# Kernel optimization log

Measured on AMD Instinct MI355X. Metric: run time of the kernel, lower is better.

The kernel has to match this reference:

```python
import jax, jax.numpy as jnp
import numpy as np

B, S, IN_DIM = 8, 1024, 512
EMBED_DIM, NUM_HEADS = 512, 8
HEAD_DIM = EMBED_DIM // NUM_HEADS
LN_EPS = 1e-5


def setup_inputs() -> dict:
    key = jax.random.key(0)
    k1, k2, k3 = jax.random.split(key, 3)
    x = jax.random.normal(k1, (B, S, IN_DIM), dtype=jnp.float32)
    # xavier_uniform for qkv_proj.weight [3*embed, in] and o_proj.weight [embed, embed]
    lim_qkv = float(np.sqrt(6.0 / (3 * EMBED_DIM + IN_DIM)))
    w_qkv = jax.random.uniform(k2, (3 * EMBED_DIM, IN_DIM), dtype=jnp.float32,
                               minval=-lim_qkv, maxval=lim_qkv)
    lim_o = float(np.sqrt(6.0 / (EMBED_DIM + EMBED_DIM)))
    w_o = jax.random.uniform(k3, (EMBED_DIM, EMBED_DIM), dtype=jnp.float32,
                             minval=-lim_o, maxval=lim_o)
    return {"x": x, "w_qkv": w_qkv, "w_o": w_o}


def reference(x, w_qkv, w_o):
    b, s, _ = x.shape
    # fused QKV projection: [b, s, 3*embed]
    qkv = jnp.einsum('bsi,ei->bse', x, w_qkv)
    # [b, h, s, 3*head_dim]
    qkv = qkv.reshape(b, s, NUM_HEADS, 3 * HEAD_DIM).transpose(0, 2, 1, 3)
    q, k, v = jnp.split(qkv, 3, axis=-1)
    scale = 1.0 / np.sqrt(HEAD_DIM)
    logits = jnp.einsum('bhqd,bhkd->bhqk', q, k) * scale  # [b, h, s, s]
    attn = jax.nn.softmax(logits, axis=-1)
    vals = jnp.einsum('bhqk,bhkd->bhqd', attn, v)
    vals = vals.transpose(0, 2, 1, 3).reshape(b, s, EMBED_DIM)
    o = jnp.einsum('bse,fe->bsf', vals, w_o)
    # LayerNorm over [seq, embed] jointly (fresh nn.LayerNorm([N, D]): weight=1, bias=0)
    mu = jnp.mean(o, axis=(-2, -1), keepdims=True)
    var = jnp.var(o, axis=(-2, -1), keepdims=True)
    o = (o - mu) / jnp.sqrt(var + LN_EPS)
    return o
```

## Files before the change

kernel.cpp:

```cpp
#include <hip/hip_runtime.h>
#include <hip/hip_bf16.h>
#include <math.h>

#define BB 8
#define SS 1024
#define INDIM 512
#define ED 512
#define NH 8
#define HD 64

typedef __attribute__((ext_vector_type(8))) short short8;
typedef __attribute__((ext_vector_type(4))) float f32x4;
typedef __attribute__((ext_vector_type(16))) float f32x16;
typedef unsigned short u16;

static __device__ __forceinline__ u16 f2bf(float f) {
  union { float f; unsigned u; } v; v.f = f;
  unsigned r = v.u + 0x7fffu + ((v.u >> 16) & 1u);
  return (u16)(r >> 16);
}

static __device__ __forceinline__ unsigned cvt_pk_bf16(float a, float b) {
  unsigned r;
  asm("v_cvt_pk_bf16_f32 %0, %1, %2" : "=v"(r) : "v"(a), "v"(b));
  return r;
}
static __device__ __forceinline__ float fast_exp2(float x) {
  float r; asm("v_exp_f32 %0, %1" : "=v"(r) : "v"(x)); return r;
}

__global__ void cvt_all(const float* __restrict__ x, const float* __restrict__ wq,
                        const float* __restrict__ wo, u16* __restrict__ xb,
                        u16* __restrict__ wqb, u16* __restrict__ wob) {
  const int n1 = 1048576;
  const int n2 = n1 + 196608;
  const int n3 = n2 + 65536;
  int i = blockIdx.x * blockDim.x + threadIdx.x;
  int stride = gridDim.x * blockDim.x;
  for (; i < n3; i += stride) {
    const float4* src; ushort4* dst; int j;
    if (i < n1)      { src = (const float4*)x;  dst = (ushort4*)xb;  j = i; }
    else if (i < n2) { src = (const float4*)wq; dst = (ushort4*)wqb; j = i - n1; }
    else             { src = (const float4*)wo; dst = (ushort4*)wob; j = i - n2; }
    float4 v = src[j];
    ushort4 o;
    o.x = f2bf(v.x); o.y = f2bf(v.y); o.z = f2bf(v.z); o.w = f2bf(v.w);
    dst[j] = o;
  }
}

template<int EPI>
__global__ __launch_bounds__(256, 2)
void gemm_nt(const u16* __restrict__ A, const u16* __restrict__ Bm, int K,
             float* __restrict__ outF,
             u16* __restrict__ qws, u16* __restrict__ kws, u16* __restrict__ vtws,
             float2* __restrict__ partials)
{
  __shared__ u16 As[128][72];
  __shared__ u16 Bs[128][72];
  const int tid = threadIdx.x;
  const int lane = tid & 63;
  const int wv = tid >> 6;
  const int wr = wv >> 1, wc = wv & 1;
  const int bm = blockIdx.x, bn = blockIdx.y;
  const int l15 = lane & 15, lg = lane >> 4;

  f32x4 acc[4][4];
  #pragma unroll
  for (int i = 0; i < 4; i++)
    #pragma unroll
    for (int j = 0; j < 4; j++) acc[i][j] = (f32x4){0.f, 0.f, 0.f, 0.f};

  for (int kk = 0; kk < K; kk += 64) {
    #pragma unroll
    for (int t = 0; t < 4; t++) {
      int ci = tid + t * 256;
      int row = ci >> 3, col = (ci & 7) * 8;
      uint4 va = *(const uint4*)(A + (size_t)(bm * 128 + row) * K + kk + col);
      *(uint4*)&As[row][col] = va;
      uint4 vb = *(const uint4*)(Bm + (size_t)(bn * 128 + row) * K + kk + col);
      *(uint4*)&Bs[row][col] = vb;
    }
    __syncthreads();
    #pragma unroll
    for (int kc = 0; kc < 2; kc++) {
      short8 af[4], bf[4];
      #pragma unroll
      for (int mi = 0; mi < 4; mi++)
        af[mi] = *(const short8*)&As[wr * 64 + mi * 16 + l15][kc * 32 + lg * 8];
      #pragma unroll
      for (int ni = 0; ni < 4; ni++)
        bf[ni] = *(const short8*)&Bs[wc * 64 + ni * 16 + l15][kc * 32 + lg * 8];
      #pragma unroll
      for (int mi = 0; mi < 4; mi++)
        #pragma unroll
        for (int ni = 0; ni < 4; ni++)
          acc[mi][ni] = __builtin_amdgcn_mfma_f32_16x16x32_bf16(af[mi], bf[ni], acc[mi][ni], 0, 0, 0);
    }
    __syncthreads();
  }

  #pragma unroll
  for (int mi = 0; mi < 4; mi++) {
    int rowg = bm * 128 + wr * 64 + mi * 16 + lg * 4;
    #pragma unroll
    for (int ni = 0; ni < 4; ni++) {
      int colg = bn * 128 + wc * 64 + ni * 16 + l15;
      #pragma unroll
      for (int r = 0; r < 4; r++) {
        int rg = rowg + r;
        float v = acc[mi][ni][r];
        if (EPI == 0) {
          int b = rg >> 10, s = rg & 1023;
          int h = colg / 192, c = colg - h * 192;
          int bh = b * 8 + h;
          if (c < 64)
            qws[((size_t)(bh * 1024 + s)) * 64 + c] = f2bf(v * 0.18033688f);
          else if (c < 128)
            kws[((size_t)(bh * 1024 + s)) * 64 + (c - 64)] = f2bf(v);
          else
            vtws[((size_t)(bh * 64 + (c - 128))) * 1024 + s] = f2bf(v);
        } else {
          outF[(size_t)rg * 512 + colg] = v;
        }
      }
    }
  }

  if (EPI == 1) {
    float s1 = 0.f, s2 = 0.f;
    #pragma unroll
    for (int mi = 0; mi < 4; mi++)
      #pragma unroll
      for (int ni = 0; ni < 4; ni++)
        #pragma unroll
        for (int r = 0; r < 4; r++) {
          float v = acc[mi][ni][r];
          s1 += v; s2 += v * v;
        }
    #pragma unroll
    for (int off = 1; off < 64; off <<= 1) {
      s1 += __shfl_xor(s1, off);
      s2 += __shfl_xor(s2, off);
    }
    __shared__ float r1[4], r2[4];
    if (lane == 0) { r1[wv] = s1; r2[wv] = s2; }
    __syncthreads();
    if (tid == 0) {
      float t1 = r1[0] + r1[1] + r1[2] + r1[3];
      float t2 = r2[0] + r2[1] + r2[2] + r2[3];
      partials[bm * 4 + bn] = make_float2(t1, t2);
    }
  }
}

__global__ __launch_bounds__(256, 2)
void attn_kernel(const u16* __restrict__ qws, const u16* __restrict__ kws,
                 const u16* __restrict__ vtws, u16* __restrict__ vals)
{
  __shared__ __align__(16) u16 Ksm[2][64][72];
  __shared__ __align__(16) u16 Vsm[2][64][72];
  const int tid = threadIdx.x;
  const int lane = tid & 63;
  const int wq = tid >> 6;
  const int l31 = lane & 31;
  const int hi = lane >> 5;
  const int logical = (blockIdx.x & 7) * 64 + (blockIdx.x >> 3);
  const int bh = logical >> 3;
  const int q0 = (logical & 7) * 128;

  short8 qf[4];
  {
    const u16* qp = qws + ((size_t)bh * 1024 + q0 + wq * 32 + l31) * 64 + 8 * hi;
    #pragma unroll
    for (int j = 0; j < 4; j++) qf[j] = *(const short8*)(qp + 16 * j);
  }

  const int srow = tid >> 3;
  const int sc8 = (tid & 7) * 8;
  uint4 kreg[2], vreg[2];
  {
    kreg[0] = *(const uint4*)(kws + ((size_t)bh * 1024 + srow) * 64 + sc8);
    kreg[1] = *(const uint4*)(kws + ((size_t)bh * 1024 + srow + 32) * 64 + sc8);
    vreg[0] = *(const uint4*)(vtws + ((size_t)(bh * 64 + srow)) * 1024 + sc8);
    vreg[1] = *(const uint4*)(vtws + ((size_t)(bh * 64 + srow + 32)) * 1024 + sc8);
    *(uint4*)&Ksm[0][srow][sc8] = kreg[0];
    *(uint4*)&Ksm[0][srow + 32][sc8] = kreg[1];
    *(uint4*)&Vsm[0][srow][sc8] = vreg[0];
    *(uint4*)&Vsm[0][srow + 32][sc8] = vreg[1];
  }
  __syncthreads();

  f32x16 o[2];
  #pragma unroll
  for (int r = 0; r < 16; r++) { o[0][r] = 0.f; o[1][r] = 0.f; }
  float m = -1e30f, l = 0.f;

  for (int t = 0; t < 16; t++) {
    const int cur = t & 1;
    if (t < 15) {
      int kv = (t + 1) * 64;
      kreg[0] = *(const uint4*)(kws + ((size_t)bh * 1024 + kv + srow) * 64 + sc8);
      kreg[1] = *(const uint4*)(kws + ((size_t)bh * 1024 + kv + srow + 32) * 64 + sc8);
      vreg[0] = *(const uint4*)(vtws + ((size_t)(bh * 64 + srow)) * 1024 + kv + sc8);
      vreg[1] = *(const uint4*)(vtws + ((size_t)(bh * 64 + srow + 32)) * 1024 + kv + sc8);
    }

    f32x16 stv[2];
    #pragma unroll
    for (int s2 = 0; s2 < 2; s2++) {
      f32x16 c;
      #pragma unroll
      for (int r = 0; r < 16; r++) c[r] = 0.f;
      #pragma unroll
      for (int j = 0; j < 4; j++) {
        short8 kf = *(const short8*)&Ksm[cur][s2 * 32 + l31][16 * j + 8 * hi];
        c = __builtin_amdgcn_mfma_f32_32x32x16_bf16(kf, qf[j], c, 0, 0, 0);
      }
      stv[s2] = c;
    }

    float mx[16];
    #pragma unroll
    for (int r = 0; r < 16; r++) mx[r] = fmaxf(stv[0][r], stv[1][r]);
    #pragma unroll
    for (int w = 8; w >= 1; w >>= 1)
      #pragma unroll
      for (int r = 0; r < w; r++) mx[r] = fmaxf(mx[r], mx[r + w]);
    float pm = fmaxf(mx[0], __shfl_xor(mx[0], 32));

    if (!__all(pm - m <= 10.0f)) {
      float mn = fmaxf(m, pm);
      float al = fast_exp2(m - mn);
      m = mn; l *= al;
      #pragma unroll
      for (int reg = 0; reg < 16; reg++) {
        int qrow = (reg & 3) + 8 * (reg >> 2) + 4 * hi;
        float alo = __shfl(al, qrow);
        o[0][reg] *= alo; o[1][reg] *= alo;
      }
    }

    unsigned pk[16];
    float ps[16];
    #pragma unroll
    for (int s2 = 0; s2 < 2; s2++)
      #pragma unroll
      for (int j = 0; j < 8; j++) {
        float p0 = fast_exp2(stv[s2][2 * j] - m);
        float p1 = fast_exp2(stv[s2][2 * j + 1] - m);
        ps[s2 * 8 + j] = p0 + p1;
        pk[s2 * 8 + j] = cvt_pk_bf16(p0, p1);
      }
    #pragma unroll
    for (int w = 8; w >= 1; w >>= 1)
      #pragma unroll
      for (int r = 0; r < w; r++) ps[r] += ps[r + w];
    l += ps[0] + __shfl_xor(ps[0], 32);

    short8 pa[4];
    #pragma unroll
    for (int cc = 0; cc < 4; cc++) {
      int base = (cc >> 1) * 8 + (cc & 1) * 4;
      unsigned a0 = pk[base + 0], a2 = pk[base + 2];
      unsigned a1 = pk[base + 1], a3 = pk[base + 3];
      asm volatile("v_permlane32_swap_b32 %0, %1" : "+v"(a0), "+v"(a2));
      asm volatile("v_permlane32_swap_b32 %0, %1" : "+v"(a1), "+v"(a3));
      union { unsigned u[4]; short8 s8; } uu;
      uu.u[0] = a0; uu.u[1] = a1; uu.u[2] = a2; uu.u[3] = a3;
      pa[cc] = uu.s8;
    }

    #pragma unroll
    for (int dh = 0; dh < 2; dh++)
      #pragma unroll
      for (int cc = 0; cc < 4; cc++) {
        short8 vf = *(const short8*)&Vsm[cur][dh * 32 + l31][16 * cc + 8 * hi];
        o[dh] = __builtin_amdgcn_mfma_f32_32x32x16_bf16(pa[cc], vf, o[dh], 0, 0, 0);
      }

    if (t < 15) {
      *(uint4*)&Ksm[cur ^ 1][srow][sc8] = kreg[0];
      *(uint4*)&Ksm[cur ^ 1][srow + 32][sc8] = kreg[1];
      *(uint4*)&Vsm[cur ^ 1][srow][sc8] = vreg[0];
      *(uint4*)&Vsm[cur ^ 1][srow + 32][sc8] = vreg[1];
    }
    __syncthreads();
  }

  const int b = bh >> 3, h = bh & 7;
  #pragma unroll
  for (int reg = 0; reg < 16; reg++) {
    int qrow = (reg & 3) + 8 * (reg >> 2) + 4 * hi;
    float linv = 1.0f / __shfl(l, qrow);
    size_t grow = (size_t)(b * 1024 + q0 + wq * 32 + qrow) * 512 + h * 64;
    vals[grow + l31]      = f2bf(o[0][reg] * linv);
    vals[grow + 32 + l31] = f2bf(o[1][reg] * linv);
  }
}

__global__ void ln_fin(const float2* __restrict__ partials, float* __restrict__ stats) {
  const int b = blockIdx.x;
  const int t = threadIdx.x;
  float s1 = 0.f, s2 = 0.f;
  if (t < 32) {
    float2 p = partials[b * 32 + t];
    s1 = p.x; s2 = p.y;
  }
  #pragma unroll
  for (int off = 1; off < 64; off <<= 1) {
    s1 += __shfl_xor(s1, off);
    s2 += __shfl_xor(s2, off);
  }
  if (t == 0) {
    float mu = s1 / 524288.f;
    float var = s2 / 524288.f - mu * mu;
    stats[b * 2] = mu;
    stats[b * 2 + 1] = rsqrtf(var + 1e-5f);
  }
}

__global__ void ln_norm(float* __restrict__ o, const float* __restrict__ stats) {
  int i = blockIdx.x * blockDim.x + threadIdx.x;
  int stride = gridDim.x * blockDim.x;
  for (; i < 1048576; i += stride) {
    int b = i >> 17;
    float mu = stats[b * 2], rs = stats[b * 2 + 1];
    float4 v = ((float4*)o)[i];
    v.x = (v.x - mu) * rs; v.y = (v.y - mu) * rs;
    v.z = (v.z - mu) * rs; v.w = (v.w - mu) * rs;
    ((float4*)o)[i] = v;
  }
}

extern "C" void kernel_launch(void* const* d_in, const int* in_sizes, int n_in,
                              void* d_out, int out_size, void* d_ws, size_t ws_size,
                              hipStream_t stream) {
  const float* x = (const float*)d_in[0];
  const float* wqkv = (const float*)d_in[1];
  const float* wo = (const float*)d_in[2];
  float* out = (float*)d_out;
  char* ws = (char*)d_ws;

  u16* xb        = (u16*)(ws + 0);
  u16* wqb       = (u16*)(ws + 8388608);
  u16* wob       = (u16*)(ws + 9961472);
  u16* qws       = (u16*)(ws + 10485760);
  u16* kws       = (u16*)(ws + 18874368);
  u16* vtws      = (u16*)(ws + 27262976);
  u16* vals      = (u16*)(ws + 35651584);
  float* st      = (float*)(ws + 44040192);
  float2* parts  = (float2*)(ws + 44040256);

  cvt_all<<<1280, 256, 0, stream>>>(x, wqkv, wo, xb, wqb, wob);

  dim3 g1(64, 12);
  gemm_nt<0><<<g1, 256, 0, stream>>>(xb, wqb, 512, nullptr, qws, kws, vtws, nullptr);

  attn_kernel<<<512, 256, 0, stream>>>(qws, kws, vtws, vals);

  dim3 g2(64, 4);
  gemm_nt<1><<<g2, 256, 0, stream>>>(vals, wob, 512, out, nullptr, nullptr, nullptr, parts);

  ln_fin<<<8, 64, 0, stream>>>(parts, st);
  ln_norm<<<2048, 256, 0, stream>>>(out, st);
}
```

Before: 90.56 us.

## Fuse LayerNorm into output GEMM via grid barrier; use direct-to-LDS loads

The output-projection GEMM now publishes its per-block sum and sum-of-squares, waits at a global atomic-counter barrier over all 256 blocks, then computes mean and rstd and writes normalized outputs directly. This removes the ln_fin and ln_norm kernels and the extra read and write of the fp32 output. Both GEMMs also switch to global_load_lds with an XOR-swizzled unpadded LDS tile, and the attention kernel raises wave priority around its MFMA blocks. The spin barrier assumes all 256 blocks are co-resident on the device, and the counter must be reset with a memset before each launch.

```diff
diff --git a/kernel.cpp b/kernel.cpp
--- a/kernel.cpp
+++ b/kernel.cpp
@@ -13,6 +13,9 @@
 typedef __attribute__((ext_vector_type(4))) float f32x4;
 typedef __attribute__((ext_vector_type(16))) float f32x16;
 typedef unsigned short u16;
+
+typedef __attribute__((address_space(1))) const void gv_t;
+typedef __attribute__((address_space(3))) void lv_t;
 
 static __device__ __forceinline__ u16 f2bf(float f) {
   union { float f; unsigned u; } v; v.f = f;
@@ -54,16 +57,18 @@
 void gemm_nt(const u16* __restrict__ A, const u16* __restrict__ Bm, int K,
              float* __restrict__ outF,
              u16* __restrict__ qws, u16* __restrict__ kws, u16* __restrict__ vtws,
-             float2* __restrict__ partials)
+             float* __restrict__ partials, unsigned* __restrict__ counter)
 {
-  __shared__ u16 As[128][72];
-  __shared__ u16 Bs[128][72];
+  __shared__ u16 As[128][64];
+  __shared__ u16 Bs[128][64];
   const int tid = threadIdx.x;
   const int lane = tid & 63;
   const int wv = tid >> 6;
   const int wr = wv >> 1, wc = wv & 1;
   const int bm = blockIdx.x, bn = blockIdx.y;
   const int l15 = lane & 15, lg = lane >> 4;
+  const int srow8 = lane >> 3;
+  const int sc8 = lane & 7;
 
   f32x4 acc[4][4];
   #pragma unroll
@@ -73,24 +78,29 @@
 
   for (int kk = 0; kk < K; kk += 64) {
     #pragma unroll
-    for (int t = 0; t < 4; t++) {
-      int ci = tid + t * 256;
-      int row = ci >> 3, col = (ci & 7) * 8;
-      uint4 va = *(const uint4*)(A + (size_t)(bm * 128 + row) * K + kk + col);
-      *(uint4*)&As[row][col] = va;
-      uint4 vb = *(const uint4*)(Bm + (size_t)(bn * 128 + row) * K + kk + col);
-      *(uint4*)&Bs[row][col] = vb;
+    for (int i = 0; i < 4; i++) {
+      int r0 = (i * 4 + wv) * 8;
+      int r = r0 + srow8;
+      int cs = sc8 ^ (r & 7);
+      const u16* ga = A + (size_t)(bm * 128 + r) * K + kk + cs * 8;
+      __builtin_amdgcn_global_load_lds((gv_t*)ga, (lv_t*)&As[r0][0], 16, 0, 0);
+      const u16* gb = Bm + (size_t)(bn * 128 + r) * K + kk + cs * 8;
+      __builtin_amdgcn_global_load_lds((gv_t*)gb, (lv_t*)&Bs[r0][0], 16, 0, 0);
     }
     __syncthreads();
     #pragma unroll
     for (int kc = 0; kc < 2; kc++) {
       short8 af[4], bf[4];
       #pragma unroll
-      for (int mi = 0; mi < 4; mi++)
-        af[mi] = *(const short8*)&As[wr * 64 + mi * 16 + l15][kc * 32 + lg * 8];
-      #pragma unroll
-      for (int ni = 0; ni < 4; ni++)
-        bf[ni] = *(const short8*)&Bs[wc * 64 + ni * 16 + l15][kc * 32 + lg * 8];
+      for (int mi = 0; mi < 4; mi++) {
+        int ra = wr * 64 + mi * 16 + l15;
+        af[mi] = *(const short8*)&As[ra][((kc * 4 + lg) ^ (ra & 7)) * 8];
+      }
+      #pragma unroll
+      for (int ni = 0; ni < 4; ni++) {
+        int rb = wc * 64 + ni * 16 + l15;
+        bf[ni] = *(const short8*)&Bs[rb][((kc * 4 + lg) ^ (rb & 7)) * 8];
+      }
       #pragma unroll
       for (int mi = 0; mi < 4; mi++)
         #pragma unroll
@@ -100,17 +110,17 @@
     __syncthreads();
   }
 
-  #pragma unroll
-  for (int mi = 0; mi < 4; mi++) {
-    int rowg = bm * 128 + wr * 64 + mi * 16 + lg * 4;
-    #pragma unroll
-    for (int ni = 0; ni < 4; ni++) {
-      int colg = bn * 128 + wc * 64 + ni * 16 + l15;
-      #pragma unroll
-      for (int r = 0; r < 4; r++) {
-        int rg = rowg + r;
-        float v = acc[mi][ni][r];
-        if (EPI == 0) {
+  if (EPI == 0) {
+    #pragma unroll
+    for (int mi = 0; mi < 4; mi++) {
+      int rowg = bm * 128 + wr * 64 + mi * 16 + lg * 4;
+      #pragma unroll
+      for (int ni = 0; ni < 4; ni++) {
+        int colg = bn * 128 + wc * 64 + ni * 16 + l15;
+        #pragma unroll
+        for (int r = 0; r < 4; r++) {
+          int rg = rowg + r;
+          float v = acc[mi][ni][r];
           int b = rg >> 10, s = rg & 1023;
           int h = colg / 192, c = colg - h * 192;
           int bh = b * 8 + h;
@@ -120,14 +130,10 @@
             kws[((size_t)(bh * 1024 + s)) * 64 + (c - 64)] = f2bf(v);
           else
             vtws[((size_t)(bh * 64 + (c - 128))) * 1024 + s] = f2bf(v);
-        } else {
-          outF[(size_t)rg * 512 + colg] = v;
         }
       }
     }
-  }
-
-  if (EPI == 1) {
+  } else {
     float s1 = 0.f, s2 = 0.f;
     #pragma unroll
     for (int mi = 0; mi < 4; mi++)
@@ -144,12 +150,51 @@
       s2 += __shfl_xor(s2, off);
     }
     __shared__ float r1[4], r2[4];
+    __shared__ float musr[2];
     if (lane == 0) { r1[wv] = s1; r2[wv] = s2; }
     __syncthreads();
     if (tid == 0) {
       float t1 = r1[0] + r1[1] + r1[2] + r1[3];
       float t2 = r2[0] + r2[1] + r2[2] + r2[3];
-      partials[bm * 4 + bn] = make_float2(t1, t2);
+      int pid = (bm * 4 + bn) * 2;
+      atomicExch(&partials[pid], t1);
+      atomicExch(&partials[pid + 1], t2);
+      __threadfence();
+      atomicAdd(counter, 1u);
+      while (atomicAdd(counter, 0u) < 256u) {}
+    }
+    __syncthreads();
+    if (wv == 0) {
+      float a = 0.f, c = 0.f;
+      if (lane < 32) {
+        int base = ((bm >> 3) * 32 + lane) * 2;
+        a = atomicAdd(&partials[base], 0.0f);
+        c = atomicAdd(&partials[base + 1], 0.0f);
+      }
+      #pragma unroll
+      for (int off = 1; off < 64; off <<= 1) {
+        a += __shfl_xor(a, off);
+        c += __shfl_xor(c, off);
+      }
+      if (lane == 0) {
+        float mu = a / 524288.f;
+        float var = c / 524288.f - mu * mu;
+        musr[0] = mu;
+        musr[1] = rsqrtf(var + 1e-5f);
+      }
+    }
+    __syncthreads();
+    float mu = musr[0], rs = musr[1];
+    #pragma unroll
+    for (int mi = 0; mi < 4; mi++) {
+      int rowg = bm * 128 + wr * 64 + mi * 16 + lg * 4;
+      #pragma unroll
+      for (int ni = 0; ni < 4; ni++) {
+        int colg = bn * 128 + wc * 64 + ni * 16 + l15;
+        #pragma unroll
+        for (int r = 0; r < 4; r++)
+          outF[(size_t)(rowg + r) * 512 + colg] = (acc[mi][ni][r] - mu) * rs;
+      }
     }
   }
 }
@@ -207,6 +252,7 @@
     }
 
     f32x16 stv[2];
+    __builtin_amdgcn_s_setprio(1);
     #pragma unroll
     for (int s2 = 0; s2 < 2; s2++) {
       f32x16 c;
@@ -219,6 +265,7 @@
       }
       stv[s2] = c;
     }
+    __builtin_amdgcn_s_setprio(0);
 
     float mx[16];
     #pragma unroll
@@ -271,6 +318,7 @@
       pa[cc] = uu.s8;
     }
 
+    __builtin_amdgcn_s_setprio(1);
     #pragma unroll
     for (int dh = 0; dh < 2; dh++)
       #pragma unroll
@@ -278,6 +326,7 @@
         short8 vf = *(const short8*)&Vsm[cur][dh * 32 + l31][16 * cc + 8 * hi];
         o[dh] = __builtin_amdgcn_mfma_f32_32x32x16_bf16(pa[cc], vf, o[dh], 0, 0, 0);
       }
+    __builtin_amdgcn_s_setprio(0);
 
     if (t < 15) {
       *(uint4*)&Ksm[cur ^ 1][srow][sc8] = kreg[0];
@@ -299,40 +348,6 @@
   }
 }
 
-__global__ void ln_fin(const float2* __restrict__ partials, float* __restrict__ stats) {
-  const int b = blockIdx.x;
-  const int t = threadIdx.x;
-  float s1 = 0.f, s2 = 0.f;
-  if (t < 32) {
-    float2 p = partials[b * 32 + t];
-    s1 = p.x; s2 = p.y;
-  }
-  #pragma unroll
-  for (int off = 1; off < 64; off <<= 1) {
-    s1 += __shfl_xor(s1, off);
-    s2 += __shfl_xor(s2, off);
-  }
-  if (t == 0) {
-    float mu = s1 / 524288.f;
-    float var = s2 / 524288.f - mu * mu;
-    stats[b * 2] = mu;
-    stats[b * 2 + 1] = rsqrtf(var + 1e-5f);
-  }
-}
-
-__global__ void ln_norm(float* __restrict__ o, const float* __restrict__ stats) {
-  int i = blockIdx.x * blockDim.x + threadIdx.x;
-  int stride = gridDim.x * blockDim.x;
-  for (; i < 1048576; i += stride) {
-    int b = i >> 17;
-    float mu = stats[b * 2], rs = stats[b * 2 + 1];
-    float4 v = ((float4*)o)[i];
-    v.x = (v.x - mu) * rs; v.y = (v.y - mu) * rs;
-    v.z = (v.z - mu) * rs; v.w = (v.w - mu) * rs;
-    ((float4*)o)[i] = v;
-  }
-}
-
 extern "C" void kernel_launch(void* const* d_in, const int* in_sizes, int n_in,
                               void* d_out, int out_size, void* d_ws, size_t ws_size,
                               hipStream_t stream) {
@@ -349,19 +364,18 @@
   u16* kws       = (u16*)(ws + 18874368);
   u16* vtws      = (u16*)(ws + 27262976);
   u16* vals      = (u16*)(ws + 35651584);
-  float* st      = (float*)(ws + 44040192);
-  float2* parts  = (float2*)(ws + 44040256);
+  unsigned* ctr  = (unsigned*)(ws + 44040192);
+  float* parts   = (float*)(ws + 44040256);
+
+  hipMemsetAsync(ctr, 0, 4, stream);
 
   cvt_all<<<1280, 256, 0, stream>>>(x, wqkv, wo, xb, wqb, wob);
 
   dim3 g1(64, 12);
-  gemm_nt<0><<<g1, 256, 0, stream>>>(xb, wqb, 512, nullptr, qws, kws, vtws, nullptr);
+  gemm_nt<0><<<g1, 256, 0, stream>>>(xb, wqb, 512, nullptr, qws, kws, vtws, nullptr, nullptr);
 
   attn_kernel<<<512, 256, 0, stream>>>(qws, kws, vtws, vals);
 
   dim3 g2(64, 4);
-  gemm_nt<1><<<g2, 256, 0, stream>>>(vals, wob, 512, out, nullptr, nullptr, nullptr, parts);
-
-  ln_fin<<<8, 64, 0, stream>>>(parts, st);
-  ln_norm<<<2048, 256, 0, stream>>>(out, st);
-}
+  gemm_nt<1><<<g2, 256, 0, stream>>>(vals, wob, 512, out, nullptr, nullptr, nullptr, parts, ctr);
+}
```

Result: slower. 93.96 us (+3.8%).
